# Kernel tuning notes

Measured on AMD Instinct MI355X. Metric: run time of the kernel, lower is better.

## Reference

```python
import jax, jax.numpy as jnp
import numpy as np

B, T, C = 2, 2048, 2048
N_HEAD = 16
HEAD_DIM = C // N_HEAD


def setup_inputs() -> dict:
    key = jax.random.key(0)
    ks = jax.random.split(key, 5)
    s = 1.0 / np.sqrt(C)
    return {
        "x": jax.random.normal(ks[0], (B, T, C), dtype=jnp.float32),
        "Wq": jax.random.normal(ks[1], (C, C), dtype=jnp.float32) * s,
        "bq": jnp.zeros((C,), dtype=jnp.float32),
        "Wk": jax.random.normal(ks[2], (C, C), dtype=jnp.float32) * s,
        "bk": jnp.zeros((C,), dtype=jnp.float32),
        "Wv": jax.random.normal(ks[3], (C, C), dtype=jnp.float32) * s,
        "bv": jnp.zeros((C,), dtype=jnp.float32),
        "Wp": jax.random.normal(ks[4], (C, C), dtype=jnp.float32) * s,
        "bp": jnp.zeros((C,), dtype=jnp.float32),
    }


def reference(x, Wq, bq, Wk, bk, Wv, bv, Wp, bp):
    Bx, Tx, Cx = x.shape
    # torch nn.Linear: y = x @ W.T + b
    def lin(x, W, b):
        return jnp.einsum("btc,dc->btd", x, W) + b

    def split_heads(y):  # (B,T,C) -> (B,H,T,hd)
        return y.reshape(Bx, Tx, N_HEAD, HEAD_DIM).transpose(0, 2, 1, 3)

    q = split_heads(lin(x, Wq, bq))
    k = split_heads(lin(x, Wk, bk))
    v = split_heads(lin(x, Wv, bv))

    scale = 1.0 / np.sqrt(HEAD_DIM).astype(np.float32)
    attn = jnp.einsum("bhqd,bhkd->bhqk", q, k) * scale  # (B,H,T,T)
    causal = jnp.tril(jnp.ones((Tx, Tx), dtype=bool))
    attn = jnp.where(causal[None, None], attn, -jnp.inf)
    attn = jax.nn.softmax(attn, axis=-1)
    out = jnp.einsum("bhqk,bhkd->bhqd", attn, v)  # (B,H,T,hd)
    # Faithful to original: transpose(-2,-1) swaps T and head_dim, then
    # a contiguous view reinterprets memory as (B,T,C).
    out = out.transpose(0, 1, 3, 2).reshape(Bx, Tx, Cx)
    return lin(out, Wp, bp)
```

## Files before the change

### kernel.cpp

```cpp
#include <hip/hip_runtime.h>
#include <stdint.h>

#define DEVI __device__ __forceinline__

typedef __attribute__((ext_vector_type(8))) short short8;
typedef __attribute__((ext_vector_type(4))) float f32x4;
typedef __attribute__((ext_vector_type(4))) unsigned int u32x4;

static constexpr int Bn = 2;
static constexpr int Tn = 2048;
static constexpr int Cn = 2048;
static constexpr int NH = 16;
static constexpr int HD = 128;
static constexpr int Kdim = 2048;

DEVI unsigned short f2bf(float f) {
  union { float f; unsigned u; } v; v.f = f;
  return (unsigned short)((v.u + 0x7FFFu + ((v.u >> 16) & 1u)) >> 16);
}

DEVI void gload_lds16(const void* g, void* l) {
  __builtin_amdgcn_global_load_lds(
      (const __attribute__((address_space(1))) void*)g,
      (__attribute__((address_space(3))) void*)l, 16, 0, 0);
}

__global__ __launch_bounds__(256) void cast_bf16_kernel(
    const float* __restrict__ src, unsigned short* __restrict__ dst, int n) {
  int idx = (blockIdx.x * blockDim.x + threadIdx.x) * 4;
  const int stride = gridDim.x * blockDim.x * 4;
  for (; idx < n; idx += stride) {
    f32x4 f = *(const f32x4*)(src + idx);
    unsigned short o[4];
    o[0] = f2bf(f[0]); o[1] = f2bf(f[1]); o[2] = f2bf(f[2]); o[3] = f2bf(f[3]);
    *(unsigned long long*)(dst + idx) = *(const unsigned long long*)o;
  }
}

__global__ __launch_bounds__(256) void cast4_kernel(
    const float* __restrict__ s0, const float* __restrict__ s1,
    const float* __restrict__ s2, const float* __restrict__ s3,
    unsigned short* __restrict__ d0, unsigned short* __restrict__ d1,
    unsigned short* __restrict__ d2, unsigned short* __restrict__ d3, int n) {
  const int w = blockIdx.y;
  const float* src = (w == 0) ? s0 : (w == 1) ? s1 : (w == 2) ? s2 : s3;
  unsigned short* dst = (w == 0) ? d0 : (w == 1) ? d1 : (w == 2) ? d2 : d3;
  int idx = (blockIdx.x * blockDim.x + threadIdx.x) * 4;
  const int stride = gridDim.x * blockDim.x * 4;
  for (; idx < n; idx += stride) {
    f32x4 f = *(const f32x4*)(src + idx);
    unsigned short o[4];
    o[0] = f2bf(f[0]); o[1] = f2bf(f[1]); o[2] = f2bf(f[2]); o[3] = f2bf(f[3]);
    *(unsigned long long*)(dst + idx) = *(const unsigned long long*)o;
  }
}

__global__ __launch_bounds__(256) void gemm_qkv_fused_kernel(
    const unsigned short* __restrict__ X,
    const unsigned short* __restrict__ Wq_, const unsigned short* __restrict__ Wk_,
    const unsigned short* __restrict__ Wv_,
    const float* __restrict__ bq_, const float* __restrict__ bk_, const float* __restrict__ bv_,
    unsigned short* __restrict__ Qo, unsigned short* __restrict__ Ko,
    unsigned short* __restrict__ Vo) {
  __shared__ unsigned short As[128 * 32];
  __shared__ unsigned short Bs[128 * 32];
  const int tid = threadIdx.x;
  const int wave = tid >> 6, lane = tid & 63;
  const int wm = wave >> 1, wn = wave & 1;
  const int quad = lane >> 4, lr = lane & 15;

  const int nidx = blockIdx.x;
  const int m0 = blockIdx.y * 128;
  const int sel = nidx >> 4;
  const int n0 = (nidx & 15) * 128;
  const unsigned short* W = (sel == 0) ? Wq_ : (sel == 1) ? Wk_ : Wv_;
  const float* bias = (sel == 0) ? bq_ : (sel == 1) ? bk_ : bv_;

  f32x4 acc[4][4];
  const f32x4 zero4 = {0.f, 0.f, 0.f, 0.f};
#pragma unroll
  for (int i = 0; i < 4; ++i)
#pragma unroll
    for (int j = 0; j < 4; ++j) acc[i][j] = zero4;

  const int srow = tid >> 2;
  const int scol = (((tid & 3) ^ ((srow >> 1) & 3)) * 8);
  const unsigned short* Ag = X + (size_t)(m0 + srow) * Kdim + scol;
  const unsigned short* Bg = W + (size_t)(n0 + srow) * Kdim + scol;
  unsigned short* Al = &As[tid * 8];
  unsigned short* Bl = &Bs[tid * 8];
  const int fsw = (quad ^ ((lr >> 1) & 3)) * 8;

  for (int k0 = 0; k0 < Kdim; k0 += 32) {
    gload_lds16(Ag + k0, Al);
    gload_lds16(Ag + (size_t)64 * Kdim + k0, Al + 2048);
    gload_lds16(Bg + k0, Bl);
    gload_lds16(Bg + (size_t)64 * Kdim + k0, Bl + 2048);
    __syncthreads();
    short8 af[4], bf[4];
#pragma unroll
    for (int mi = 0; mi < 4; ++mi)
      af[mi] = *(const short8*)&As[(wm * 64 + mi * 16 + lr) * 32 + fsw];
#pragma unroll
    for (int ni = 0; ni < 4; ++ni)
      bf[ni] = *(const short8*)&Bs[(wn * 64 + ni * 16 + lr) * 32 + fsw];
#pragma unroll
    for (int mi = 0; mi < 4; ++mi)
#pragma unroll
      for (int ni = 0; ni < 4; ++ni)
        acc[mi][ni] = __builtin_amdgcn_mfma_f32_16x16x32_bf16(af[mi], bf[ni], acc[mi][ni], 0, 0, 0);
    __syncthreads();
  }

  if (sel == 2) {
#pragma unroll
    for (int ni = 0; ni < 4; ++ni) {
      const int n = n0 + wn * 64 + ni * 16 + lr;
      const float bv = bias[n];
      const int h = n >> 7, d = n & 127;
#pragma unroll
      for (int mi = 0; mi < 4; ++mi) {
        const int m = m0 + wm * 64 + mi * 16 + quad * 4;
        const int b = m >> 11, t = m & 2047;
        unsigned short o4[4];
#pragma unroll
        for (int r = 0; r < 4; ++r) o4[r] = f2bf(acc[mi][ni][r] + bv);
        *(unsigned long long*)&Vo[(((size_t)(b * NH + h)) * HD + d) * Tn + t] =
            *(const unsigned long long*)o4;
      }
    }
  } else {
    unsigned short* Out = (sel == 0) ? Qo : Ko;
#pragma unroll
    for (int ni = 0; ni < 4; ++ni) {
      const int n = n0 + wn * 64 + ni * 16 + lr;
      const float bv = bias[n];
      const int h = n >> 7, d = n & 127;
#pragma unroll
      for (int mi = 0; mi < 4; ++mi) {
#pragma unroll
        for (int r = 0; r < 4; ++r) {
          const int m = m0 + wm * 64 + mi * 16 + quad * 4 + r;
          const int b = m >> 11, t = m & 2047;
          Out[(((size_t)(b * NH + h)) * Tn + t) * HD + d] = f2bf(acc[mi][ni][r] + bv);
        }
      }
    }
  }
}

__global__ __launch_bounds__(256) void gemm_proj_kernel(
    const unsigned short* __restrict__ Aall,
    const unsigned short* __restrict__ W,
    const float* __restrict__ bias,
    float* __restrict__ Y) {
  __shared__ unsigned short As[128 * 32];
  __shared__ unsigned short Bs[128 * 32];
  const int tid = threadIdx.x;
  const int wave = tid >> 6, lane = tid & 63;
  const int wm = wave >> 1, wn = wave & 1;
  const int quad = lane >> 4, lr = lane & 15;

  const int m0 = blockIdx.y * 128, n0 = blockIdx.x * 128;
  const int bz = blockIdx.z;
  const unsigned short* A = Aall + (size_t)bz * Cn * Tn;

  f32x4 acc[4][4];
  const f32x4 zero4 = {0.f, 0.f, 0.f, 0.f};
#pragma unroll
  for (int i = 0; i < 4; ++i)
#pragma unroll
    for (int j = 0; j < 4; ++j) acc[i][j] = zero4;

  const int srow = tid >> 2;
  const int scol = (((tid & 3) ^ ((srow >> 1) & 3)) * 8);
  const unsigned short* Ag = A + (size_t)(m0 + srow) * Kdim + scol;
  const unsigned short* Bg = W + (size_t)(n0 + srow) * Kdim + scol;
  unsigned short* Al = &As[tid * 8];
  unsigned short* Bl = &Bs[tid * 8];
  const int fsw = (quad ^ ((lr >> 1) & 3)) * 8;

  for (int k0 = 0; k0 < Kdim; k0 += 32) {
    gload_lds16(Ag + k0, Al);
    gload_lds16(Ag + (size_t)64 * Kdim + k0, Al + 2048);
    gload_lds16(Bg + k0, Bl);
    gload_lds16(Bg + (size_t)64 * Kdim + k0, Bl + 2048);
    __syncthreads();
    short8 af[4], bf[4];
#pragma unroll
    for (int mi = 0; mi < 4; ++mi)
      af[mi] = *(const short8*)&As[(wm * 64 + mi * 16 + lr) * 32 + fsw];
#pragma unroll
    for (int ni = 0; ni < 4; ++ni)
      bf[ni] = *(const short8*)&Bs[(wn * 64 + ni * 16 + lr) * 32 + fsw];
#pragma unroll
    for (int mi = 0; mi < 4; ++mi)
#pragma unroll
      for (int ni = 0; ni < 4; ++ni)
        acc[mi][ni] = __builtin_amdgcn_mfma_f32_16x16x32_bf16(af[mi], bf[ni], acc[mi][ni], 0, 0, 0);
    __syncthreads();
  }

#pragma unroll
  for (int ni = 0; ni < 4; ++ni) {
    const int n = n0 + wn * 64 + ni * 16 + lr;
    const float bv = bias[n];
#pragma unroll
    for (int mi = 0; mi < 4; ++mi) {
#pragma unroll
      for (int r = 0; r < 4; ++r) {
        const int m = m0 + wm * 64 + mi * 16 + quad * 4 + r;
        Y[((size_t)bz * Tn + m) * Cn + n] = acc[mi][ni][r] + bv;
      }
    }
  }
}

__global__ __launch_bounds__(256, 1) void attn_kernel(
    const unsigned short* __restrict__ Q,
    const unsigned short* __restrict__ K,
    const unsigned short* __restrict__ V,
    unsigned short* __restrict__ Ot) {
  constexpr int KST = 136;
  constexpr int VST = 136;
  constexpr int PST = 136;
  __shared__ unsigned short Ks[128 * KST];
  __shared__ unsigned short Vs[144 * VST];
  __shared__ unsigned short Ps[128 * PST];

  const int tid = threadIdx.x;
  const int wave = tid >> 6, lane = tid & 63;
  const int quad = lane >> 4, lr = lane & 15;
  const int bh = blockIdx.y;
  const float SL = 0.08838834764831845f * 1.4426950408889634f;

  const unsigned short* Kp = K + (size_t)bh * Tn * HD;
  const unsigned short* Vp = V + (size_t)bh * HD * Tn;
  unsigned short* Pw = &Ps[wave * 32 * PST];

  for (int i = tid; i < 16 * VST; i += 256) Vs[128 * VST + i] = 0x3F80;

  const f32x4 zero4 = {0.f, 0.f, 0.f, 0.f};
#pragma unroll 1
  for (int half = 0; half < 2; ++half) {
    const int jt = half ? (15 - (int)blockIdx.x) : (int)blockIdx.x;
    const int q0 = jt * 128;

    const unsigned short* Qp = Q + ((size_t)bh * Tn + q0 + wave * 32) * HD;
    short8 qf[2][4];
#pragma unroll
    for (int mi = 0; mi < 2; ++mi)
#pragma unroll
      for (int ks = 0; ks < 4; ++ks)
        qf[mi][ks] = *(const short8*)&Qp[(mi * 16 + lr) * HD + ks * 32 + quad * 8];

    f32x4 oacc[2][9];
#pragma unroll
    for (int mi = 0; mi < 2; ++mi)
#pragma unroll
      for (int nd = 0; nd < 9; ++nd) oacc[mi][nd] = zero4;

    const int nch = q0 / 128 + 1;
    for (int c = 0; c < nch; ++c) {
      const int k0 = c * 128;
      {
        const int r = tid >> 1;
        const int cc = (tid & 1) * 64;
        const unsigned short* kg = &Kp[(size_t)(k0 + r) * HD + cc];
        const unsigned short* vg = &Vp[(size_t)r * Tn + k0 + cc];
        unsigned short* kl = &Ks[r * KST + cc];
        unsigned short* vl = &Vs[r * VST + cc];
#pragma unroll
        for (int p = 0; p < 8; ++p) {
          *(u32x4*)(kl + p * 8) = *(const u32x4*)(kg + p * 8);
          *(u32x4*)(vl + p * 8) = *(const u32x4*)(vg + p * 8);
        }
      }
      __syncthreads();

      f32x4 sa[2][8];
#pragma unroll
      for (int mi = 0; mi < 2; ++mi)
#pragma unroll
        for (int nt = 0; nt < 8; ++nt) sa[mi][nt] = zero4;
#pragma unroll
      for (int nt = 0; nt < 8; ++nt) {
        short8 kf[4];
#pragma unroll
        for (int ks = 0; ks < 4; ++ks)
          kf[ks] = *(const short8*)&Ks[(nt * 16 + lr) * KST + ks * 32 + quad * 8];
#pragma unroll
        for (int mi = 0; mi < 2; ++mi)
#pragma unroll
          for (int ks = 0; ks < 4; ++ks)
            sa[mi][nt] = __builtin_amdgcn_mfma_f32_16x16x32_bf16(qf[mi][ks], kf[ks], sa[mi][nt], 0, 0, 0);
      }

      if (k0 == q0) {
#pragma unroll
        for (int mi = 0; mi < 2; ++mi)
#pragma unroll
          for (int nt = 0; nt < 8; ++nt)
#pragma unroll
            for (int r = 0; r < 4; ++r) {
              const int qg = q0 + wave * 32 + mi * 16 + quad * 4 + r;
              const int kg = k0 + nt * 16 + lr;
              if (kg > qg) sa[mi][nt][r] = -3.0e38f;
            }
      }

#pragma unroll
      for (int mi = 0; mi < 2; ++mi)
#pragma unroll
        for (int nt = 0; nt < 8; ++nt)
#pragma unroll
          for (int r = 0; r < 4; ++r) {
            const float p = __builtin_amdgcn_exp2f(sa[mi][nt][r] * SL);
            Pw[(mi * 16 + quad * 4 + r) * PST + nt * 16 + lr] = f2bf(p);
          }

#pragma unroll
      for (int kt = 0; kt < 4; ++kt) {
        short8 pf[2];
#pragma unroll
        for (int mi = 0; mi < 2; ++mi)
          pf[mi] = *(const short8*)&Pw[(mi * 16 + lr) * PST + kt * 32 + quad * 8];
#pragma unroll
        for (int nd = 0; nd < 9; ++nd) {
          short8 vf = *(const short8*)&Vs[(nd * 16 + lr) * VST + kt * 32 + quad * 8];
#pragma unroll
          for (int mi = 0; mi < 2; ++mi)
            oacc[mi][nd] = __builtin_amdgcn_mfma_f32_16x16x32_bf16(pf[mi], vf, oacc[mi][nd], 0, 0, 0);
        }
      }
      __syncthreads();
    }

#pragma unroll
    for (int mi = 0; mi < 2; ++mi)
#pragma unroll
      for (int r = 0; r < 4; ++r) {
        const float rl = 1.0f / oacc[mi][8][r];
        const int tl = wave * 32 + mi * 16 + quad * 4 + r;
#pragma unroll
        for (int nd = 0; nd < 8; ++nd)
          Ps[tl * PST + nd * 16 + lr] = f2bf(oacc[mi][nd][r] * rl);
      }
    __syncthreads();
    {
      unsigned short* Od = Ot + (size_t)bh * HD * Tn + q0;
#pragma unroll
      for (int p = 0; p < 8; ++p) {
        const int d = p * 16 + (tid >> 4);
        const int t8 = (tid & 15) * 8;
        alignas(16) unsigned short v[8];
#pragma unroll
        for (int j = 0; j < 8; ++j) v[j] = Ps[(t8 + j) * PST + d];
        *(u32x4*)&Od[(size_t)d * Tn + t8] = *(const u32x4*)v;
      }
    }
    __syncthreads();
  }
}

extern "C" void kernel_launch(void* const* d_in, const int* in_sizes, int n_in,
                              void* d_out, int out_size, void* d_ws, size_t ws_size,
                              hipStream_t stream) {
  const float* x  = (const float*)d_in[0];
  const float* Wq = (const float*)d_in[1];
  const float* bq = (const float*)d_in[2];
  const float* Wk = (const float*)d_in[3];
  const float* bk = (const float*)d_in[4];
  const float* Wv = (const float*)d_in[5];
  const float* bv = (const float*)d_in[6];
  const float* Wp = (const float*)d_in[7];
  const float* bp = (const float*)d_in[8];
  float* out = (float*)d_out;

  char* ws = (char*)d_ws;
  const size_t MB = 1ull << 20;
  unsigned short* Xbf = (unsigned short*)(ws);
  unsigned short* Wqb = (unsigned short*)(ws + 16 * MB);
  unsigned short* Wkb = (unsigned short*)(ws + 24 * MB);
  unsigned short* Wvb = (unsigned short*)(ws + 32 * MB);
  unsigned short* Wpb = (unsigned short*)(ws + 40 * MB);
  unsigned short* Qb  = (unsigned short*)(ws + 48 * MB);
  unsigned short* Kb  = (unsigned short*)(ws + 64 * MB);
  unsigned short* Vtb = (unsigned short*)(ws + 80 * MB);
  unsigned short* Otb = (unsigned short*)(ws + 96 * MB);

  cast_bf16_kernel<<<dim3(1024), dim3(256), 0, stream>>>(x, Xbf, Bn * Tn * Cn);
  cast4_kernel<<<dim3(512, 4), dim3(256), 0, stream>>>(
      Wq, Wk, Wv, Wp, Wqb, Wkb, Wvb, Wpb, Cn * Cn);

  gemm_qkv_fused_kernel<<<dim3(48, 32), dim3(256), 0, stream>>>(
      Xbf, Wqb, Wkb, Wvb, bq, bk, bv, Qb, Kb, Vtb);

  attn_kernel<<<dim3(8, Bn * NH), dim3(256), 0, stream>>>(Qb, Kb, Vtb, Otb);

  gemm_proj_kernel<<<dim3(16, 16, 2), dim3(256), 0, stream>>>(Otb, Wpb, bp, out);
}
```

Baseline: 441.2 us.

## Rewrite QKV GEMM as 256x256 tile, 8-wave, double-buffered phased pipeline

Replaces the 128x128 single-buffered QKV projection GEMM with a 512-thread 256x256-tile kernel. It uses K=64 steps, double-buffered LDS, and four interleaved phases per step that issue the next tile's global-to-LDS loads between MFMA groups under s_setprio. It also adds XOR-swizzled LDS layout and block-index swizzling for L2 locality. This removes the per-step full-stall load/compute serialization and raises data reuse per tile. The cost is 128KB of LDS per block and heavy register use, which limits occupancy, and only 384 blocks for the device.

```diff
diff --git a/kernel.cpp b/kernel.cpp
--- a/kernel.cpp
+++ b/kernel.cpp
@@ -55,62 +55,136 @@
   }
 }
 
-__global__ __launch_bounds__(256) void gemm_qkv_fused_kernel(
+#define QKV_BAR() __builtin_amdgcn_s_barrier()
+#define QKV_MFMA(d, a, b) d = __builtin_amdgcn_mfma_f32_16x16x32_bf16(a, b, d, 0, 0, 0)
+
+__global__ __launch_bounds__(512, 2) void gemm_qkv_8ph_kernel(
     const unsigned short* __restrict__ X,
     const unsigned short* __restrict__ Wq_, const unsigned short* __restrict__ Wk_,
     const unsigned short* __restrict__ Wv_,
     const float* __restrict__ bq_, const float* __restrict__ bk_, const float* __restrict__ bv_,
     unsigned short* __restrict__ Qo, unsigned short* __restrict__ Ko,
     unsigned short* __restrict__ Vo) {
-  __shared__ unsigned short As[128 * 32];
-  __shared__ unsigned short Bs[128 * 32];
+  constexpr int NT = Kdim / 64;
+  __shared__ unsigned short L[2][2][16384];
+
   const int tid = threadIdx.x;
   const int wave = tid >> 6, lane = tid & 63;
-  const int wm = wave >> 1, wn = wave & 1;
+  const int wm = wave >> 2, wn = wave & 3;
   const int quad = lane >> 4, lr = lane & 15;
 
-  const int nidx = blockIdx.x;
-  const int m0 = blockIdx.y * 128;
-  const int sel = nidx >> 4;
-  const int n0 = (nidx & 15) * 128;
+  const int flat = (int)blockIdx.x + 24 * (int)blockIdx.y;
+  const int swz = (flat & 7) * 48 + (flat >> 3);
+  const int bx = swz % 24, by = swz / 24;
+  const int sel = bx >> 3;
+  const int n0 = (bx & 7) * 256;
+  const int m0 = by * 256;
   const unsigned short* W = (sel == 0) ? Wq_ : (sel == 1) ? Wk_ : Wv_;
   const float* bias = (sel == 0) ? bq_ : (sel == 1) ? bk_ : bv_;
 
-  f32x4 acc[4][4];
+  f32x4 acc[8][4];
   const f32x4 zero4 = {0.f, 0.f, 0.f, 0.f};
 #pragma unroll
-  for (int i = 0; i < 4; ++i)
+  for (int i = 0; i < 8; ++i)
 #pragma unroll
     for (int j = 0; j < 4; ++j) acc[i][j] = zero4;
 
-  const int srow = tid >> 2;
-  const int scol = (((tid & 3) ^ ((srow >> 1) & 3)) * 8);
-  const unsigned short* Ag = X + (size_t)(m0 + srow) * Kdim + scol;
-  const unsigned short* Bg = W + (size_t)(n0 + srow) * Kdim + scol;
-  unsigned short* Al = &As[tid * 8];
-  unsigned short* Bl = &Bs[tid * 8];
-  const int fsw = (quad ^ ((lr >> 1) & 3)) * 8;
-
-  for (int k0 = 0; k0 < Kdim; k0 += 32) {
-    gload_lds16(Ag + k0, Al);
-    gload_lds16(Ag + (size_t)64 * Kdim + k0, Al + 2048);
-    gload_lds16(Bg + k0, Bl);
-    gload_lds16(Bg + (size_t)64 * Kdim + k0, Bl + 2048);
-    __syncthreads();
-    short8 af[4], bf[4];
-#pragma unroll
-    for (int mi = 0; mi < 4; ++mi)
-      af[mi] = *(const short8*)&As[(wm * 64 + mi * 16 + lr) * 32 + fsw];
-#pragma unroll
-    for (int ni = 0; ni < 4; ++ni)
-      bf[ni] = *(const short8*)&Bs[(wn * 64 + ni * 16 + lr) * 32 + fsw];
-#pragma unroll
-    for (int mi = 0; mi < 4; ++mi)
-#pragma unroll
-      for (int ni = 0; ni < 4; ++ni)
-        acc[mi][ni] = __builtin_amdgcn_mfma_f32_16x16x32_bf16(af[mi], bf[ni], acc[mi][ni], 0, 0, 0);
-    __syncthreads();
-  }
+  const int srow = tid >> 3;
+  const int schunk = (tid & 7) ^ (srow & 7);
+  const unsigned short* Asrc = X + (size_t)(m0 + srow) * Kdim + schunk * 8;
+  const unsigned short* Bsrc = W + (size_t)(n0 + srow) * Kdim + schunk * 8;
+
+  auto STAGE_A = [&](int buf, int h, int t) {
+    unsigned short* d = &L[buf][0][h * 8192 + tid * 8];
+    const unsigned short* s = Asrc + (size_t)(h * 128) * Kdim + t * 64;
+    gload_lds16(s, d);
+    gload_lds16(s + (size_t)64 * Kdim, d + 4096);
+  };
+  auto STAGE_B = [&](int buf, int h, int t) {
+    unsigned short* d = &L[buf][1][h * 8192 + tid * 8];
+    const unsigned short* s = Bsrc + (size_t)(h * 128) * Kdim + t * 64;
+    gload_lds16(s, d);
+    gload_lds16(s + (size_t)64 * Kdim, d + 4096);
+  };
+
+  const int pc0 = (quad) ^ (lr & 7);
+  const int pc1 = (4 + quad) ^ (lr & 7);
+  const int aoff = (wm * 128 + lr) * 64;
+  const int boff = (wn * 64 + lr) * 64;
+#define RDA(mi, pc) (*(const short8*)&L[cur][0][aoff + (mi) * 1024 + (pc) * 8])
+#define RDB(ni, pc) (*(const short8*)&L[cur][1][boff + (ni) * 1024 + (pc) * 8])
+
+  STAGE_A(0, 0, 0); STAGE_A(0, 1, 0);
+  STAGE_B(0, 0, 0); STAGE_B(0, 1, 0);
+  STAGE_B(1, 0, 1); STAGE_B(1, 1, 1);
+  asm volatile("s_waitcnt vmcnt(4)" ::: "memory");
+  QKV_BAR();
+
+  short8 Af[4][2], B01[2][2], B23[2][2];
+
+  for (int t = 0; t < NT; ++t) {
+    const int cur = t & 1, nxt = cur ^ 1;
+#pragma unroll
+    for (int m = 0; m < 4; ++m) { Af[m][0] = RDA(m, pc0); Af[m][1] = RDA(m, pc1); }
+#pragma unroll
+    for (int n = 0; n < 2; ++n) { B01[n][0] = RDB(n, pc0); B01[n][1] = RDB(n, pc1); }
+    if (t + 1 < NT) STAGE_A(nxt, 0, t + 1);
+    QKV_BAR();
+    __builtin_amdgcn_s_setprio(1);
+#pragma unroll
+    for (int m = 0; m < 4; ++m)
+#pragma unroll
+      for (int n = 0; n < 2; ++n) {
+        QKV_MFMA(acc[m][n], Af[m][0], B01[n][0]);
+        QKV_MFMA(acc[m][n], Af[m][1], B01[n][1]);
+      }
+    __builtin_amdgcn_s_setprio(0);
+    QKV_BAR();
+#pragma unroll
+    for (int n = 0; n < 2; ++n) { B23[n][0] = RDB(n + 2, pc0); B23[n][1] = RDB(n + 2, pc1); }
+    if (t + 1 < NT) STAGE_A(nxt, 1, t + 1);
+    QKV_BAR();
+    __builtin_amdgcn_s_setprio(1);
+#pragma unroll
+    for (int m = 0; m < 4; ++m)
+#pragma unroll
+      for (int n = 0; n < 2; ++n) {
+        QKV_MFMA(acc[m][n + 2], Af[m][0], B23[n][0]);
+        QKV_MFMA(acc[m][n + 2], Af[m][1], B23[n][1]);
+      }
+    __builtin_amdgcn_s_setprio(0);
+    QKV_BAR();
+#pragma unroll
+    for (int m = 0; m < 4; ++m) { Af[m][0] = RDA(m + 4, pc0); Af[m][1] = RDA(m + 4, pc1); }
+    if (t + 2 < NT) STAGE_B(cur, 0, t + 2);
+    QKV_BAR();
+    __builtin_amdgcn_s_setprio(1);
+#pragma unroll
+    for (int m = 0; m < 4; ++m)
+#pragma unroll
+      for (int n = 0; n < 2; ++n) {
+        QKV_MFMA(acc[m + 4][n], Af[m][0], B01[n][0]);
+        QKV_MFMA(acc[m + 4][n], Af[m][1], B01[n][1]);
+      }
+    __builtin_amdgcn_s_setprio(0);
+    QKV_BAR();
+    if (t + 2 < NT) STAGE_B(cur, 1, t + 2);
+    QKV_BAR();
+    __builtin_amdgcn_s_setprio(1);
+#pragma unroll
+    for (int m = 0; m < 4; ++m)
+#pragma unroll
+      for (int n = 0; n < 2; ++n) {
+        QKV_MFMA(acc[m + 4][n + 2], Af[m][0], B23[n][0]);
+        QKV_MFMA(acc[m + 4][n + 2], Af[m][1], B23[n][1]);
+      }
+    __builtin_amdgcn_s_setprio(0);
+    if (t < NT - 2) { asm volatile("s_waitcnt vmcnt(4)" ::: "memory"); }
+    else            { asm volatile("s_waitcnt vmcnt(0)" ::: "memory"); }
+    QKV_BAR();
+  }
+#undef RDA
+#undef RDB
 
   if (sel == 2) {
 #pragma unroll
@@ -119,13 +193,13 @@
       const float bv = bias[n];
       const int h = n >> 7, d = n & 127;
 #pragma unroll
-      for (int mi = 0; mi < 4; ++mi) {
-        const int m = m0 + wm * 64 + mi * 16 + quad * 4;
-        const int b = m >> 11, t = m & 2047;
+      for (int mi = 0; mi < 8; ++mi) {
+        const int m = m0 + wm * 128 + mi * 16 + quad * 4;
+        const int b = m >> 11, tt = m & 2047;
         unsigned short o4[4];
 #pragma unroll
         for (int r = 0; r < 4; ++r) o4[r] = f2bf(acc[mi][ni][r] + bv);
-        *(unsigned long long*)&Vo[(((size_t)(b * NH + h)) * HD + d) * Tn + t] =
+        *(unsigned long long*)&Vo[(((size_t)(b * NH + h)) * HD + d) * Tn + tt] =
             *(const unsigned long long*)o4;
       }
     }
@@ -137,12 +211,12 @@
       const float bv = bias[n];
       const int h = n >> 7, d = n & 127;
 #pragma unroll
-      for (int mi = 0; mi < 4; ++mi) {
+      for (int mi = 0; mi < 8; ++mi) {
 #pragma unroll
         for (int r = 0; r < 4; ++r) {
-          const int m = m0 + wm * 64 + mi * 16 + quad * 4 + r;
-          const int b = m >> 11, t = m & 2047;
-          Out[(((size_t)(b * NH + h)) * Tn + t) * HD + d] = f2bf(acc[mi][ni][r] + bv);
+          const int m = m0 + wm * 128 + mi * 16 + quad * 4 + r;
+          const int b = m >> 11, tt = m & 2047;
+          Out[(((size_t)(b * NH + h)) * Tn + tt) * HD + d] = f2bf(acc[mi][ni][r] + bv);
         }
       }
     }
@@ -393,7 +467,7 @@
   cast4_kernel<<<dim3(512, 4), dim3(256), 0, stream>>>(
       Wq, Wk, Wv, Wp, Wqb, Wkb, Wvb, Wpb, Cn * Cn);
 
-  gemm_qkv_fused_kernel<<<dim3(48, 32), dim3(256), 0, stream>>>(
+  gemm_qkv_8ph_kernel<<<dim3(24, 16), dim3(512), 0, stream>>>(
       Xbf, Wqb, Wkb, Wvb, bq, bk, bv, Qb, Kb, Vtb);
 
   attn_kernel<<<dim3(8, Bn * NH), dim3(256), 0, stream>>>(Qb, Kb, Vtb, Otb);
```

Measured after the change: 428.6 us. 2.9% less time.

## Rewrite GEMMs as double-buffered 256x128 tiles and prefetch attention K/V into registers

Applied to the files above, without the earlier changes.

Both the QKV and projection GEMMs move to a shared 512-thread 256x128 tile core. It uses double-buffered LDS, BK=64 with XOR swizzle, staged async global-to-LDS loads interleaved with two MFMA phases, s_setprio around the MFMA blocks, and a block-index swizzle meant to improve L2 locality. The attention kernel now prefetches the next K/V chunk into registers while computing the current one, hiding global load latency behind compute. The cost is heavier LDS use (96KB per block), more registers and hand-tuned vmcnt waits that must match the load ordering exactly.

```diff
diff --git a/kernel.cpp b/kernel.cpp
--- a/kernel.cpp
+++ b/kernel.cpp
@@ -55,161 +55,173 @@
   }
 }
 
-__global__ __launch_bounds__(256) void gemm_qkv_fused_kernel(
+#define G_BAR() __builtin_amdgcn_s_barrier()
+#define G_MFMA(d, a, b) d = __builtin_amdgcn_mfma_f32_16x16x32_bf16(a, b, d, 0, 0, 0)
+
+#define GEMM_CORE_256x128(Asrc_, Bsrc_)                                          \
+  f32x4 acc[8][2];                                                               \
+  const f32x4 zero4 = {0.f, 0.f, 0.f, 0.f};                                      \
+  _Pragma("unroll") for (int i = 0; i < 8; ++i)                                  \
+      _Pragma("unroll") for (int j = 0; j < 2; ++j) acc[i][j] = zero4;           \
+  const int srow = tid >> 3;                                                     \
+  const int schunk = (tid & 7) ^ (srow & 7);                                     \
+  const unsigned short* Asrc = (Asrc_) + (size_t)srow * Kdim + schunk * 8;       \
+  const unsigned short* Bsrc = (Bsrc_) + (size_t)srow * Kdim + schunk * 8;       \
+  auto STAGE_A = [&](int buf, int h, int t) {                                    \
+    unsigned short* d = &L[buf][h * 8192 + tid * 8];                             \
+    const unsigned short* s = Asrc + (size_t)(h * 128) * Kdim + t * 64;          \
+    gload_lds16(s, d);                                                           \
+    gload_lds16(s + (size_t)64 * Kdim, d + 4096);                                \
+  };                                                                             \
+  auto STAGE_B = [&](int buf, int t) {                                           \
+    unsigned short* d = &L[buf][16384 + tid * 8];                                \
+    const unsigned short* s = Bsrc + t * 64;                                     \
+    gload_lds16(s, d);                                                           \
+    gload_lds16(s + (size_t)64 * Kdim, d + 4096);                                \
+  };                                                                             \
+  const int pc0 = (quad) ^ (lr & 7);                                             \
+  const int pc1 = (4 + quad) ^ (lr & 7);                                         \
+  const int aoff = (wm * 128 + lr) * 64;                                         \
+  const int boff = 16384 + (wn * 32 + lr) * 64;                                  \
+  STAGE_A(0, 0, 0); STAGE_A(0, 1, 0);                                            \
+  STAGE_B(0, 0);                                                                 \
+  STAGE_B(1, 1);                                                                 \
+  asm volatile("s_waitcnt vmcnt(2)" ::: "memory");                               \
+  G_BAR();                                                                       \
+  short8 Af[4][2], Bf[2][2];                                                     \
+  for (int t = 0; t < NT; ++t) {                                                 \
+    const int cur = t & 1, nxt = cur ^ 1;                                        \
+    _Pragma("unroll") for (int m = 0; m < 4; ++m) {                              \
+      Af[m][0] = *(const short8*)&L[cur][aoff + m * 1024 + pc0 * 8];             \
+      Af[m][1] = *(const short8*)&L[cur][aoff + m * 1024 + pc1 * 8];             \
+    }                                                                            \
+    _Pragma("unroll") for (int n = 0; n < 2; ++n) {                              \
+      Bf[n][0] = *(const short8*)&L[cur][boff + n * 1024 + pc0 * 8];             \
+      Bf[n][1] = *(const short8*)&L[cur][boff + n * 1024 + pc1 * 8];             \
+    }                                                                            \
+    if (t + 1 < NT) STAGE_A(nxt, 0, t + 1);                                      \
+    G_BAR();                                                                     \
+    __builtin_amdgcn_s_setprio(1);                                               \
+    _Pragma("unroll") for (int m = 0; m < 4; ++m)                                \
+        _Pragma("unroll") for (int n = 0; n < 2; ++n) {                          \
+      G_MFMA(acc[m][n], Af[m][0], Bf[n][0]);                                     \
+      G_MFMA(acc[m][n], Af[m][1], Bf[n][1]);                                     \
+    }                                                                            \
+    __builtin_amdgcn_s_setprio(0);                                               \
+    G_BAR();                                                                     \
+    _Pragma("unroll") for (int m = 0; m < 4; ++m) {                              \
+      Af[m][0] = *(const short8*)&L[cur][aoff + (m + 4) * 1024 + pc0 * 8];       \
+      Af[m][1] = *(const short8*)&L[cur][aoff + (m + 4) * 1024 + pc1 * 8];       \
+    }                                                                            \
+    if (t + 1 < NT) STAGE_A(nxt, 1, t + 1);                                      \
+    if (t + 2 < NT) STAGE_B(cur, t + 2);                                         \
+    G_BAR();                                                                     \
+    __builtin_amdgcn_s_setprio(1);                                               \
+    _Pragma("unroll") for (int m = 0; m < 4; ++m)                                \
+        _Pragma("unroll") for (int n = 0; n < 2; ++n) {                          \
+      G_MFMA(acc[m + 4][n], Af[m][0], Bf[n][0]);                                 \
+      G_MFMA(acc[m + 4][n], Af[m][1], Bf[n][1]);                                 \
+    }                                                                            \
+    __builtin_amdgcn_s_setprio(0);                                               \
+    if (t < NT - 2) { asm volatile("s_waitcnt vmcnt(2)" ::: "memory"); }         \
+    else            { asm volatile("s_waitcnt vmcnt(0)" ::: "memory"); }         \
+    G_BAR();                                                                     \
+  }
+
+__global__ __launch_bounds__(512, 2) void gemm_qkv_256x128_kernel(
     const unsigned short* __restrict__ X,
     const unsigned short* __restrict__ Wq_, const unsigned short* __restrict__ Wk_,
     const unsigned short* __restrict__ Wv_,
     const float* __restrict__ bq_, const float* __restrict__ bk_, const float* __restrict__ bv_,
     unsigned short* __restrict__ Qo, unsigned short* __restrict__ Ko,
     unsigned short* __restrict__ Vo) {
-  __shared__ unsigned short As[128 * 32];
-  __shared__ unsigned short Bs[128 * 32];
+  constexpr int NT = Kdim / 64;
+  __shared__ unsigned short L[2][24576];
+
   const int tid = threadIdx.x;
   const int wave = tid >> 6, lane = tid & 63;
-  const int wm = wave >> 1, wn = wave & 1;
+  const int wm = wave >> 2, wn = wave & 3;
   const int quad = lane >> 4, lr = lane & 15;
 
-  const int nidx = blockIdx.x;
-  const int m0 = blockIdx.y * 128;
-  const int sel = nidx >> 4;
-  const int n0 = (nidx & 15) * 128;
+  const int flat = (int)blockIdx.x + 48 * (int)blockIdx.y;
+  const int swz = (flat & 7) * 96 + (flat >> 3);
+  const int bx = swz % 48, by = swz / 48;
+  const int sel = bx >> 4;
+  const int nw0 = (bx & 15) * 128;
+  const int m0 = by * 256;
   const unsigned short* W = (sel == 0) ? Wq_ : (sel == 1) ? Wk_ : Wv_;
   const float* bias = (sel == 0) ? bq_ : (sel == 1) ? bk_ : bv_;
 
-  f32x4 acc[4][4];
-  const f32x4 zero4 = {0.f, 0.f, 0.f, 0.f};
-#pragma unroll
-  for (int i = 0; i < 4; ++i)
-#pragma unroll
-    for (int j = 0; j < 4; ++j) acc[i][j] = zero4;
-
-  const int srow = tid >> 2;
-  const int scol = (((tid & 3) ^ ((srow >> 1) & 3)) * 8);
-  const unsigned short* Ag = X + (size_t)(m0 + srow) * Kdim + scol;
-  const unsigned short* Bg = W + (size_t)(n0 + srow) * Kdim + scol;
-  unsigned short* Al = &As[tid * 8];
-  unsigned short* Bl = &Bs[tid * 8];
-  const int fsw = (quad ^ ((lr >> 1) & 3)) * 8;
-
-  for (int k0 = 0; k0 < Kdim; k0 += 32) {
-    gload_lds16(Ag + k0, Al);
-    gload_lds16(Ag + (size_t)64 * Kdim + k0, Al + 2048);
-    gload_lds16(Bg + k0, Bl);
-    gload_lds16(Bg + (size_t)64 * Kdim + k0, Bl + 2048);
-    __syncthreads();
-    short8 af[4], bf[4];
-#pragma unroll
-    for (int mi = 0; mi < 4; ++mi)
-      af[mi] = *(const short8*)&As[(wm * 64 + mi * 16 + lr) * 32 + fsw];
-#pragma unroll
-    for (int ni = 0; ni < 4; ++ni)
-      bf[ni] = *(const short8*)&Bs[(wn * 64 + ni * 16 + lr) * 32 + fsw];
-#pragma unroll
-    for (int mi = 0; mi < 4; ++mi)
-#pragma unroll
-      for (int ni = 0; ni < 4; ++ni)
-        acc[mi][ni] = __builtin_amdgcn_mfma_f32_16x16x32_bf16(af[mi], bf[ni], acc[mi][ni], 0, 0, 0);
-    __syncthreads();
-  }
+  GEMM_CORE_256x128(X + (size_t)m0 * Kdim, W + (size_t)nw0 * Kdim)
 
   if (sel == 2) {
 #pragma unroll
-    for (int ni = 0; ni < 4; ++ni) {
-      const int n = n0 + wn * 64 + ni * 16 + lr;
+    for (int ni = 0; ni < 2; ++ni) {
+      const int n = nw0 + wn * 32 + ni * 16 + lr;
       const float bv = bias[n];
       const int h = n >> 7, d = n & 127;
 #pragma unroll
-      for (int mi = 0; mi < 4; ++mi) {
-        const int m = m0 + wm * 64 + mi * 16 + quad * 4;
-        const int b = m >> 11, t = m & 2047;
+      for (int mi = 0; mi < 8; ++mi) {
+        const int m = m0 + wm * 128 + mi * 16 + quad * 4;
+        const int b = m >> 11, tt = m & 2047;
         unsigned short o4[4];
 #pragma unroll
         for (int r = 0; r < 4; ++r) o4[r] = f2bf(acc[mi][ni][r] + bv);
-        *(unsigned long long*)&Vo[(((size_t)(b * NH + h)) * HD + d) * Tn + t] =
+        *(unsigned long long*)&Vo[(((size_t)(b * NH + h)) * HD + d) * Tn + tt] =
             *(const unsigned long long*)o4;
       }
     }
   } else {
     unsigned short* Out = (sel == 0) ? Qo : Ko;
 #pragma unroll
-    for (int ni = 0; ni < 4; ++ni) {
-      const int n = n0 + wn * 64 + ni * 16 + lr;
+    for (int ni = 0; ni < 2; ++ni) {
+      const int n = nw0 + wn * 32 + ni * 16 + lr;
       const float bv = bias[n];
       const int h = n >> 7, d = n & 127;
 #pragma unroll
-      for (int mi = 0; mi < 4; ++mi) {
+      for (int mi = 0; mi < 8; ++mi) {
 #pragma unroll
         for (int r = 0; r < 4; ++r) {
-          const int m = m0 + wm * 64 + mi * 16 + quad * 4 + r;
-          const int b = m >> 11, t = m & 2047;
-          Out[(((size_t)(b * NH + h)) * Tn + t) * HD + d] = f2bf(acc[mi][ni][r] + bv);
+          const int m = m0 + wm * 128 + mi * 16 + quad * 4 + r;
+          const int b = m >> 11, tt = m & 2047;
+          Out[(((size_t)(b * NH + h)) * Tn + tt) * HD + d] = f2bf(acc[mi][ni][r] + bv);
         }
       }
     }
   }
 }
 
-__global__ __launch_bounds__(256) void gemm_proj_kernel(
+__global__ __launch_bounds__(512, 2) void gemm_proj_256x128_kernel(
     const unsigned short* __restrict__ Aall,
-    const unsigned short* __restrict__ W,
+    const unsigned short* __restrict__ Wp_,
     const float* __restrict__ bias,
     float* __restrict__ Y) {
-  __shared__ unsigned short As[128 * 32];
-  __shared__ unsigned short Bs[128 * 32];
+  constexpr int NT = Kdim / 64;
+  __shared__ unsigned short L[2][24576];
+
   const int tid = threadIdx.x;
   const int wave = tid >> 6, lane = tid & 63;
-  const int wm = wave >> 1, wn = wave & 1;
+  const int wm = wave >> 2, wn = wave & 3;
   const int quad = lane >> 4, lr = lane & 15;
 
-  const int m0 = blockIdx.y * 128, n0 = blockIdx.x * 128;
+  const int flat = (int)blockIdx.x + 16 * (int)blockIdx.y;
+  const int swz = (flat & 7) * 16 + (flat >> 3);
+  const int bx = swz % 16, by = swz / 16;
+  const int m0 = by * 256, n0 = bx * 128;
   const int bz = blockIdx.z;
   const unsigned short* A = Aall + (size_t)bz * Cn * Tn;
 
-  f32x4 acc[4][4];
-  const f32x4 zero4 = {0.f, 0.f, 0.f, 0.f};
-#pragma unroll
-  for (int i = 0; i < 4; ++i)
-#pragma unroll
-    for (int j = 0; j < 4; ++j) acc[i][j] = zero4;
-
-  const int srow = tid >> 2;
-  const int scol = (((tid & 3) ^ ((srow >> 1) & 3)) * 8);
-  const unsigned short* Ag = A + (size_t)(m0 + srow) * Kdim + scol;
-  const unsigned short* Bg = W + (size_t)(n0 + srow) * Kdim + scol;
-  unsigned short* Al = &As[tid * 8];
-  unsigned short* Bl = &Bs[tid * 8];
-  const int fsw = (quad ^ ((lr >> 1) & 3)) * 8;
-
-  for (int k0 = 0; k0 < Kdim; k0 += 32) {
-    gload_lds16(Ag + k0, Al);
-    gload_lds16(Ag + (size_t)64 * Kdim + k0, Al + 2048);
-    gload_lds16(Bg + k0, Bl);
-    gload_lds16(Bg + (size_t)64 * Kdim + k0, Bl + 2048);
-    __syncthreads();
-    short8 af[4], bf[4];
-#pragma unroll
-    for (int mi = 0; mi < 4; ++mi)
-      af[mi] = *(const short8*)&As[(wm * 64 + mi * 16 + lr) * 32 + fsw];
-#pragma unroll
-    for (int ni = 0; ni < 4; ++ni)
-      bf[ni] = *(const short8*)&Bs[(wn * 64 + ni * 16 + lr) * 32 + fsw];
-#pragma unroll
-    for (int mi = 0; mi < 4; ++mi)
-#pragma unroll
-      for (int ni = 0; ni < 4; ++ni)
-        acc[mi][ni] = __builtin_amdgcn_mfma_f32_16x16x32_bf16(af[mi], bf[ni], acc[mi][ni], 0, 0, 0);
-    __syncthreads();
-  }
-
-#pragma unroll
-  for (int ni = 0; ni < 4; ++ni) {
-    const int n = n0 + wn * 64 + ni * 16 + lr;
+  GEMM_CORE_256x128(A + (size_t)m0 * Kdim, Wp_ + (size_t)n0 * Kdim)
+
+#pragma unroll
+  for (int ni = 0; ni < 2; ++ni) {
+    const int n = n0 + wn * 32 + ni * 16 + lr;
     const float bv = bias[n];
 #pragma unroll
-    for (int mi = 0; mi < 4; ++mi) {
+    for (int mi = 0; mi < 8; ++mi) {
 #pragma unroll
       for (int r = 0; r < 4; ++r) {
-        const int m = m0 + wm * 64 + mi * 16 + quad * 4 + r;
+        const int m = m0 + wm * 128 + mi * 16 + quad * 4 + r;
         Y[((size_t)bz * Tn + m) * Cn + n] = acc[mi][ni][r] + bv;
       }
     }
@@ -240,6 +252,12 @@
 
   for (int i = tid; i < 16 * VST; i += 256) Vs[128 * VST + i] = 0x3F80;
 
+  const int r = tid >> 1;
+  const int cc = (tid & 1) * 64;
+  unsigned short* kl = &Ks[r * KST + cc];
+  unsigned short* vl = &Vs[r * VST + cc];
+  u32x4 kreg[8], vreg[8];
+
   const f32x4 zero4 = {0.f, 0.f, 0.f, 0.f};
 #pragma unroll 1
   for (int half = 0; half < 2; ++half) {
@@ -261,22 +279,35 @@
       for (int nd = 0; nd < 9; ++nd) oacc[mi][nd] = zero4;
 
     const int nch = q0 / 128 + 1;
+
+    {
+      const unsigned short* kg = &Kp[(size_t)r * HD + cc];
+      const unsigned short* vg = &Vp[(size_t)r * Tn + cc];
+#pragma unroll
+      for (int p = 0; p < 8; ++p) {
+        kreg[p] = *(const u32x4*)(kg + p * 8);
+        vreg[p] = *(const u32x4*)(vg + p * 8);
+      }
+    }
+
     for (int c = 0; c < nch; ++c) {
       const int k0 = c * 128;
-      {
-        const int r = tid >> 1;
-        const int cc = (tid & 1) * 64;
-        const unsigned short* kg = &Kp[(size_t)(k0 + r) * HD + cc];
-        const unsigned short* vg = &Vp[(size_t)r * Tn + k0 + cc];
-        unsigned short* kl = &Ks[r * KST + cc];
-        unsigned short* vl = &Vs[r * VST + cc];
+#pragma unroll
+      for (int p = 0; p < 8; ++p) {
+        *(u32x4*)(kl + p * 8) = kreg[p];
+        *(u32x4*)(vl + p * 8) = vreg[p];
+      }
+      __syncthreads();
+      if (c + 1 < nch) {
+        const int k1 = k0 + 128;
+        const unsigned short* kg = &Kp[(size_t)(k1 + r) * HD + cc];
+        const unsigned short* vg = &Vp[(size_t)r * Tn + k1 + cc];
 #pragma unroll
         for (int p = 0; p < 8; ++p) {
-          *(u32x4*)(kl + p * 8) = *(const u32x4*)(kg + p * 8);
-          *(u32x4*)(vl + p * 8) = *(const u32x4*)(vg + p * 8);
+          kreg[p] = *(const u32x4*)(kg + p * 8);
+          vreg[p] = *(const u32x4*)(vg + p * 8);
         }
       }
-      __syncthreads();
 
       f32x4 sa[2][8];
 #pragma unroll
@@ -302,10 +333,10 @@
 #pragma unroll
           for (int nt = 0; nt < 8; ++nt)
 #pragma unroll
-            for (int r = 0; r < 4; ++r) {
-              const int qg = q0 + wave * 32 + mi * 16 + quad * 4 + r;
+            for (int r2 = 0; r2 < 4; ++r2) {
+              const int qg = q0 + wave * 32 + mi * 16 + quad * 4 + r2;
               const int kg = k0 + nt * 16 + lr;
-              if (kg > qg) sa[mi][nt][r] = -3.0e38f;
+              if (kg > qg) sa[mi][nt][r2] = -3.0e38f;
             }
       }
 
@@ -314,9 +345,9 @@
 #pragma unroll
         for (int nt = 0; nt < 8; ++nt)
 #pragma unroll
-          for (int r = 0; r < 4; ++r) {
-            const float p = __builtin_amdgcn_exp2f(sa[mi][nt][r] * SL);
-            Pw[(mi * 16 + quad * 4 + r) * PST + nt * 16 + lr] = f2bf(p);
+          for (int r2 = 0; r2 < 4; ++r2) {
+            const float p = __builtin_amdgcn_exp2f(sa[mi][nt][r2] * SL);
+            Pw[(mi * 16 + quad * 4 + r2) * PST + nt * 16 + lr] = f2bf(p);
           }
 
 #pragma unroll
@@ -339,12 +370,12 @@
 #pragma unroll
     for (int mi = 0; mi < 2; ++mi)
 #pragma unroll
-      for (int r = 0; r < 4; ++r) {
-        const float rl = 1.0f / oacc[mi][8][r];
-        const int tl = wave * 32 + mi * 16 + quad * 4 + r;
+      for (int r2 = 0; r2 < 4; ++r2) {
+        const float rl = 1.0f / oacc[mi][8][r2];
+        const int tl = wave * 32 + mi * 16 + quad * 4 + r2;
 #pragma unroll
         for (int nd = 0; nd < 8; ++nd)
-          Ps[tl * PST + nd * 16 + lr] = f2bf(oacc[mi][nd][r] * rl);
+          Ps[tl * PST + nd * 16 + lr] = f2bf(oacc[mi][nd][r2] * rl);
       }
     __syncthreads();
     {
@@ -393,10 +424,11 @@
   cast4_kernel<<<dim3(512, 4), dim3(256), 0, stream>>>(
       Wq, Wk, Wv, Wp, Wqb, Wkb, Wvb, Wpb, Cn * Cn);
 
-  gemm_qkv_fused_kernel<<<dim3(48, 32), dim3(256), 0, stream>>>(
+  gemm_qkv_256x128_kernel<<<dim3(48, 16), dim3(512), 0, stream>>>(
       Xbf, Wqb, Wkb, Wvb, bq, bk, bv, Qb, Kb, Vtb);
 
   attn_kernel<<<dim3(8, Bn * NH), dim3(256), 0, stream>>>(Qb, Kb, Vtb, Otb);
 
-  gemm_proj_kernel<<<dim3(16, 16, 2), dim3(256), 0, stream>>>(Otb, Wpb, bp, out);
-}
+  gemm_proj_256x128_kernel<<<dim3(16, 8, 2), dim3(512), 0, stream>>>(
+      Otb, Wpb, bp, out);
+}
```

Result: faster. 410.5 us (-7.0%).
